# Kernel optimization log

Measured on AMD Instinct MI355X. Metric: run time of the kernel, lower is better.

The kernel has to match this reference:

```python
import jax, jax.numpy as jnp
import numpy as np

B, N, C_IN, C_OUT, K, E = 32, 1024, 64, 64, 3, 16
H1, M1 = 16, 2  # hyperGNN_dim, middle_dim (same for fc and fc1)


def setup_inputs() -> dict:
    key = jax.random.key(0)
    ks = jax.random.split(key, 20)
    rn = lambda k, shape, s=1.0: jax.random.normal(k, shape, jnp.float32) * s
    return {
        "x": rn(ks[0], (B, N, C_IN)),
        "node_emb0": rn(ks[1], (B, N, E)),
        "node_emb1": rn(ks[2], (N, E)),
        "time": rn(ks[3], (B, N, 1)),
        "day": rn(ks[4], (B, N, 1)),
        "speed": rn(ks[5], (B, N, 1)),
        "occupy": rn(ks[6], (B, N, 1)),
        # fc: dim_in -> 16 -> 2 -> embed_dim
        "fc_w1": rn(ks[7], (H1, C_IN), 0.1), "fc_b1": jnp.zeros((H1,), jnp.float32),
        "fc_w2": rn(ks[8], (M1, H1), 0.1), "fc_b2": jnp.zeros((M1,), jnp.float32),
        "fc_w3": rn(ks[9], (E, M1), 0.1), "fc_b3": jnp.zeros((E,), jnp.float32),
        # fc1: 1 -> 16 -> 2 -> embed_dim
        "fc1_w1": rn(ks[10], (H1, 1), 0.1), "fc1_b1": jnp.zeros((H1,), jnp.float32),
        "fc1_w2": rn(ks[11], (M1, H1), 0.1), "fc1_b2": jnp.zeros((M1,), jnp.float32),
        "fc1_w3": rn(ks[12], (E, M1), 0.1), "fc1_b3": jnp.zeros((E,), jnp.float32),
        "alpha": jnp.array([0.6], jnp.float32),
        "beta": jnp.array([0.4], jnp.float32),
        "weights_pool": rn(ks[13], (E, K, C_IN, C_OUT), 0.02),
        "backward_weights_pool": rn(ks[14], (E, K, C_IN, C_OUT), 0.02),
        "bias_pool": rn(ks[15], (E, C_OUT), 0.02),
        "weights1": rn(ks[16], (C_IN, C_OUT), 0.02),
        "att_w": rn(ks[17], (1, C_IN), 0.1),
        "att_b": jnp.zeros((1,), jnp.float32),
    }


def _mlp(x, w1, b1, w2, b2, w3, b3):
    h = jax.nn.sigmoid(x @ w1.T + b1)
    h = jax.nn.sigmoid(h @ w2.T + b2)
    return h @ w3.T + b3


def _attn_pool(xg, att_w, att_b, weights1):
    # xg: [B, K, N, C]
    nf = xg.mean(axis=1)                       # [B, N, C]
    scores = nf @ att_w.T + att_b              # [B, N, 1]
    aw = jax.nn.softmax(scores, axis=1)        # softmax over nodes
    gf = jnp.sum(nf * aw, axis=1)              # [B, C]
    return (gf @ weights1)[:, None, :]         # [B, 1, C_OUT], broadcasts over N


def reference(x, node_emb0, node_emb1, time, day, speed, occupy,
              fc_w1, fc_b1, fc_w2, fc_b2, fc_w3, fc_b3,
              fc1_w1, fc1_b1, fc1_w2, fc1_b2, fc1_w3, fc1_b3,
              alpha, beta, weights_pool, backward_weights_pool,
              bias_pool, weights1, att_w, att_b):
    k_steps = weights_pool.shape[1]
    # hypernetwork filters
    filt = _mlp(x, fc_w1, fc_b1, fc_w2, fc_b2, fc_w3, fc_b3)           # [B,N,E]
    f1 = _mlp(speed, fc1_w1, fc1_b1, fc1_w2, fc1_b2, fc1_w3, fc1_b3)   # [B,N,E]
    f2 = _mlp(occupy, fc1_w1, fc1_b1, fc1_w2, fc1_b2, fc1_w3, fc1_b3)  # [B,N,E]
    nv = jnp.tanh(node_emb0 * filt)
    nv = jnp.tanh(nv * f1)
    nv = jnp.tanh(nv * f2)
    supports = jax.nn.relu(jnp.einsum('bme,bne->bmn', nv, nv))          # [B,N,N]
    # forward diffusion
    xs = [x]
    for _ in range(1, k_steps):
        xs.append(jax.nn.leaky_relu(jnp.einsum('bmn,bnc->bmc', supports, xs[-1])))
    xg1 = jnp.stack(xs, axis=1)                                         # [B,K,N,C]
    gf = _attn_pool(xg1, att_w, att_b, weights1)                        # [B,1,O]
    w_fwd = jnp.einsum('ne,ekio->nkio', node_emb1, weights_pool)        # [N,K,C,O]
    # backward diffusion (starts from last forward step, uses A^T)
    s_t = jnp.swapaxes(supports, 1, 2)
    xb = [xs[-1]]
    for _ in range(1, k_steps):
        xb.append(jax.nn.leaky_relu(jnp.einsum('bmn,bnc->bmc', s_t, xb[-1])))
    xg2 = jnp.stack(xb, axis=1)                                         # [B,K,N,C]
    gf1 = _attn_pool(xg2, att_w, att_b, weights1)                       # [B,1,O]
    w_bwd = jnp.einsum('ne,ekio->nkio', node_emb1, backward_weights_pool)
    bias = node_emb1 @ bias_pool                                        # [N,O]
    d1 = jnp.einsum('bkni,nkio->bno', xg1, w_fwd)
    d2 = jnp.einsum('bkni,nkio->bno', xg2, w_bwd)
    return alpha * d1 + beta * d2 + bias + gf + gf1
```

## Files before the change

### kernel.cpp

```cpp
#include <hip/hip_runtime.h>
#include <cmath>

#define NB 32
#define NN 1024
#define NC 64
#define NE 16

typedef _Float16 f16;
typedef __attribute__((ext_vector_type(2))) _Float16 f16x2;
typedef __attribute__((ext_vector_type(4))) _Float16 f16x4;
typedef __attribute__((ext_vector_type(8))) _Float16 f16x8;
typedef __attribute__((ext_vector_type(16))) float f32x16;

#define NVSTR 24
#define SSTR  40
#define XSTR  40
#define ASTR  40

__device__ __forceinline__ float sigm(float v) { return 1.0f / (1.0f + expf(-v)); }
__device__ __forceinline__ float lrelu(float v) { return v > 0.0f ? v : 0.01f * v; }

__global__ __launch_bounds__(64) void nv_kernel(
    const float* __restrict__ x, const float* __restrict__ emb0,
    const float* __restrict__ speed, const float* __restrict__ occupy,
    const float* __restrict__ fw1, const float* __restrict__ fb1,
    const float* __restrict__ fw2, const float* __restrict__ fb2,
    const float* __restrict__ fw3, const float* __restrict__ fb3,
    const float* __restrict__ gw1, const float* __restrict__ gb1,
    const float* __restrict__ gw2, const float* __restrict__ gb2,
    const float* __restrict__ gw3, const float* __restrict__ gb3,
    float* __restrict__ nv_out)
{
    const int row = blockIdx.x * 64 + threadIdx.x;

    float h1[16];
    #pragma unroll
    for (int j = 0; j < 16; ++j) h1[j] = fb1[j];
    {
        const float4* xr = reinterpret_cast<const float4*>(x + (size_t)row * 64);
        #pragma unroll
        for (int i4 = 0; i4 < 16; ++i4) {
            float4 xv = xr[i4];
            #pragma unroll
            for (int j = 0; j < 16; ++j) {
                const float* wr = fw1 + j * 64 + i4 * 4;
                h1[j] += xv.x * wr[0] + xv.y * wr[1] + xv.z * wr[2] + xv.w * wr[3];
            }
        }
    }
    #pragma unroll
    for (int j = 0; j < 16; ++j) h1[j] = sigm(h1[j]);

    float h2a = fb2[0], h2b = fb2[1];
    #pragma unroll
    for (int j = 0; j < 16; ++j) { h2a += h1[j] * fw2[j]; h2b += h1[j] * fw2[16 + j]; }
    h2a = sigm(h2a); h2b = sigm(h2b);

    const float sp = speed[row], oc = occupy[row];
    float ga = gb2[0], gb_ = gb2[1];
    float oa = gb2[0], ob_ = gb2[1];
    #pragma unroll
    for (int j = 0; j < 16; ++j) {
        float g1 = sigm(sp * gw1[j] + gb1[j]);
        float o1 = sigm(oc * gw1[j] + gb1[j]);
        ga += g1 * gw2[j];  gb_ += g1 * gw2[16 + j];
        oa += o1 * gw2[j];  ob_ += o1 * gw2[16 + j];
    }
    ga = sigm(ga); gb_ = sigm(gb_); oa = sigm(oa); ob_ = sigm(ob_);

    const float* e0 = emb0 + (size_t)row * 16;
    float vout[16];
    #pragma unroll
    for (int j = 0; j < 16; ++j) {
        float filt = h2a * fw3[j * 2] + h2b * fw3[j * 2 + 1] + fb3[j];
        float f1v  = ga  * gw3[j * 2] + gb_ * gw3[j * 2 + 1] + gb3[j];
        float f2v  = oa  * gw3[j * 2] + ob_ * gw3[j * 2 + 1] + gb3[j];
        float v = tanhf(e0[j] * filt);
        v = tanhf(v * f1v);
        v = tanhf(v * f2v);
        vout[j] = v;
    }
    float4* dst = reinterpret_cast<float4*>(nv_out + (size_t)row * 16);
    #pragma unroll
    for (int q = 0; q < 4; ++q) {
        float4 o; o.x = vout[4 * q]; o.y = vout[4 * q + 1]; o.z = vout[4 * q + 2]; o.w = vout[4 * q + 3];
        dst[q] = o;
    }
}

__global__ __launch_bounds__(256) void xsplit_kernel(
    const float* __restrict__ x, f16* __restrict__ Th, f16* __restrict__ Tl)
{
    const int b = blockIdx.x;
    const int n0 = blockIdx.y * 64;
    const int t = threadIdx.x;

    __shared__ float tile[64][65];
    {
        int r = t >> 2;
        const float4* src = reinterpret_cast<const float4*>(x + ((size_t)b * NN + n0 + r) * NC);
        #pragma unroll
        for (int i = 0; i < 4; ++i) {
            int fi = (t & 3) + 4 * i;
            float4 vv = src[fi];
            tile[r][fi * 4 + 0] = vv.x; tile[r][fi * 4 + 1] = vv.y;
            tile[r][fi * 4 + 2] = vv.z; tile[r][fi * 4 + 3] = vv.w;
        }
    }
    __syncthreads();
    const int c = t & 63, ng = (t >> 6) * 16;
    f16x8 ph0, ph1, pl0, pl1;
    #pragma unroll
    for (int j = 0; j < 8; ++j) {
        float v = tile[ng + j][c];
        f16 h = (f16)v; ph0[j] = h; pl0[j] = (f16)(v - (float)h);
    }
    #pragma unroll
    for (int j = 0; j < 8; ++j) {
        float v = tile[ng + 8 + j][c];
        f16 h = (f16)v; ph1[j] = h; pl1[j] = (f16)(v - (float)h);
    }
    f16* dh = Th + ((size_t)b * NC + c) * NN + n0 + ng;
    f16* dl = Tl + ((size_t)b * NC + c) * NN + n0 + ng;
    *(f16x8*)dh = ph0; *(f16x8*)(dh + 8) = ph1;
    *(f16x8*)dl = pl0; *(f16x8*)(dl + 8) = pl1;
}

__global__ __launch_bounds__(512, 2) void sgen_fused_kernel(
    const float* __restrict__ nv,
    const f16* __restrict__ xTh, const f16* __restrict__ xTl,
    f16* __restrict__ Sh, f16* __restrict__ Sl,
    float* __restrict__ yout, f16* __restrict__ yTh, f16* __restrict__ yTl)
{
    const int b = blockIdx.x;
    const int m0 = blockIdx.y * 128;
    const int t = threadIdx.x;
    const int l = t & 63;
    const int g = l >> 5;
    const int l31 = l & 31;
    const int w = t >> 6;
    const int mq = w >> 1;
    const int nh = w & 1;

    __shared__ __align__(16) f16 nvBh[128 * NVSTR], nvBl[128 * NVSTR];
    __shared__ __align__(16) f16 Xsh[4][64 * XSTR], Xsl[4][64 * XSTR];
    __shared__ __align__(16) f16 Sth[4][128 * SSTR], Stl[4][128 * SSTR];

    const size_t sbase = (size_t)b * NN * NN;

    {
        int row = t >> 2, e0 = (t & 3) * 4;
        const float* src = nv + ((size_t)b * NN + m0 + row) * NE + e0;
        float v0 = src[0], v1 = src[1], v2 = src[2], v3 = src[3];
        f16x4 ph, pl;
        ph[0] = (f16)v0; pl[0] = (f16)(v0 - (float)ph[0]);
        ph[1] = (f16)v1; pl[1] = (f16)(v1 - (float)ph[1]);
        ph[2] = (f16)v2; pl[2] = (f16)(v2 - (float)ph[2]);
        ph[3] = (f16)v3; pl[3] = (f16)(v3 - (float)ph[3]);
        *(f16x4*)&Sth[0][row * NVSTR + e0] = ph;
        *(f16x4*)&Stl[0][row * NVSTR + e0] = pl;
    }
    __syncthreads();
    f16x8 Ah = *(const f16x8*)&Sth[0][(mq * 32 + l31) * NVSTR + g * 8];
    f16x8 Al = *(const f16x8*)&Stl[0][(mq * 32 + l31) * NVSTR + g * 8];

    f32x16 acc0, acc1;
    #pragma unroll
    for (int r = 0; r < 16; ++r) { acc0[r] = 0.0f; acc1[r] = 0.0f; }

    const int brow = t >> 2, be0 = (t & 3) * 4;
    const int xc = t >> 3, xpart = t & 7;
    const int xsub = xpart >> 1, xhalf = xpart & 1;

    for (int it = 0; it < 8; ++it) {
        {
            const float* src = nv + ((size_t)b * NN + it * 128 + brow) * NE + be0;
            float v0 = src[0], v1 = src[1], v2 = src[2], v3 = src[3];
            f16x4 ph, pl;
            ph[0] = (f16)v0; pl[0] = (f16)(v0 - (float)ph[0]);
            ph[1] = (f16)v1; pl[1] = (f16)(v1 - (float)ph[1]);
            ph[2] = (f16)v2; pl[2] = (f16)(v2 - (float)ph[2]);
            ph[3] = (f16)v3; pl[3] = (f16)(v3 - (float)ph[3]);
            *(f16x4*)&nvBh[brow * NVSTR + be0] = ph;
            *(f16x4*)&nvBl[brow * NVSTR + be0] = pl;
        }
        {
            const f16* sH = xTh + ((size_t)b * NC + xc) * NN + it * 128 + xsub * 32 + xhalf * 16;
            const f16* sL = xTl + ((size_t)b * NC + xc) * NN + it * 128 + xsub * 32 + xhalf * 16;
            *(f16x8*)&Xsh[xsub][xc * XSTR + xhalf * 16] = *(const f16x8*)sH;
            *(f16x8*)&Xsh[xsub][xc * XSTR + xhalf * 16 + 8] = *(const f16x8*)(sH + 8);
            *(f16x8*)&Xsl[xsub][xc * XSTR + xhalf * 16] = *(const f16x8*)sL;
            *(f16x8*)&Xsl[xsub][xc * XSTR + xhalf * 16 + 8] = *(const f16x8*)(sL + 8);
        }
        __syncthreads();

        #pragma unroll
        for (int tl = 0; tl < 2; ++tl) {
            const int tile = nh * 2 + tl;
            f16x8 Bh = *(const f16x8*)&nvBh[(tile * 32 + l31) * NVSTR + g * 8];
            f16x8 Bl = *(const f16x8*)&nvBl[(tile * 32 + l31) * NVSTR + g * 8];
            f32x16 sa;
            #pragma unroll
            for (int r = 0; r < 16; ++r) sa[r] = 0.0f;
            sa = __builtin_amdgcn_mfma_f32_32x32x16_f16(Al, Bh, sa, 0, 0, 0);
            sa = __builtin_amdgcn_mfma_f32_32x32x16_f16(Ah, Bl, sa, 0, 0, 0);
            sa = __builtin_amdgcn_mfma_f32_32x32x16_f16(Ah, Bh, sa, 0, 0, 0);
            const int n = it * 128 + tile * 32 + l31;
            #pragma unroll
            for (int r = 0; r < 16; ++r) {
                float vv = fmaxf(sa[r], 0.0f);
                f16 h = (f16)vv; f16 lo = (f16)(vv - (float)h);
                int mloc = mq * 32 + (r & 3) + 8 * (r >> 2) + 4 * g;
                Sh[sbase + (size_t)(m0 + mloc) * NN + n] = h;
                Sl[sbase + (size_t)(m0 + mloc) * NN + n] = lo;
                Sth[tile][mloc * SSTR + l31] = h;
                Stl[tile][mloc * SSTR + l31] = lo;
            }
        }
        __syncthreads();

        #pragma unroll
        for (int tl = 0; tl < 2; ++tl) {
            const int tile = nh * 2 + tl;
            #pragma unroll
            for (int ku = 0; ku < 2; ++ku) {
                f16x8 Ah2 = *(const f16x8*)&Sth[tile][(mq * 32 + l31) * SSTR + ku * 16 + g * 8];
                f16x8 Al2 = *(const f16x8*)&Stl[tile][(mq * 32 + l31) * SSTR + ku * 16 + g * 8];
                {
                    f16x8 Bh = *(const f16x8*)&Xsh[tile][l31 * XSTR + ku * 16 + g * 8];
                    f16x8 Bl = *(const f16x8*)&Xsl[tile][l31 * XSTR + ku * 16 + g * 8];
                    acc0 = __builtin_amdgcn_mfma_f32_32x32x16_f16(Al2, Bh, acc0, 0, 0, 0);
                    acc0 = __builtin_amdgcn_mfma_f32_32x32x16_f16(Ah2, Bl, acc0, 0, 0, 0);
                    acc0 = __builtin_amdgcn_mfma_f32_32x32x16_f16(Ah2, Bh, acc0, 0, 0, 0);
                }
                {
                    f16x8 Bh = *(const f16x8*)&Xsh[tile][(32 + l31) * XSTR + ku * 16 + g * 8];
                    f16x8 Bl = *(const f16x8*)&Xsl[tile][(32 + l31) * XSTR + ku * 16 + g * 8];
                    acc1 = __builtin_amdgcn_mfma_f32_32x32x16_f16(Al2, Bh, acc1, 0, 0, 0);
                    acc1 = __builtin_amdgcn_mfma_f32_32x32x16_f16(Ah2, Bl, acc1, 0, 0, 0);
                    acc1 = __builtin_amdgcn_mfma_f32_32x32x16_f16(Ah2, Bh, acc1, 0, 0, 0);
                }
            }
        }
        __syncthreads();
    }

    float* red = reinterpret_cast<float*>(&Sth[0][0]);
    if (nh == 1) {
        #pragma unroll
        for (int r = 0; r < 16; ++r) {
            int crow = (r & 3) + 8 * (r >> 2) + 4 * g;
            red[((mq * 2 + 0) * 32 + crow) * 33 + l31] = acc0[r];
            red[((mq * 2 + 1) * 32 + crow) * 33 + l31] = acc1[r];
        }
    }
    __syncthreads();
    if (nh == 0) {
        #pragma unroll
        for (int ch = 0; ch < 2; ++ch) {
            const int colg = ch * 32 + l31;
            #pragma unroll
            for (int q = 0; q < 4; ++q) {
                float v[4];
                #pragma unroll
                for (int j = 0; j < 4; ++j) {
                    int r = q * 4 + j;
                    int crow = j + 8 * q + 4 * g;
                    float part = (ch == 0) ? acc0[r] : acc1[r];
                    v[j] = lrelu(part + red[((mq * 2 + ch) * 32 + crow) * 33 + l31]);
                }
                const int mrow = m0 + mq * 32 + 8 * q + 4 * g;
                #pragma unroll
                for (int j = 0; j < 4; ++j)
                    yout[((size_t)b * NN + mrow + j) * NC + colg] = v[j];
                f16x4 ph, pl;
                #pragma unroll
                for (int j = 0; j < 4; ++j) {
                    f16 h = (f16)v[j];
                    ph[j] = h; pl[j] = (f16)(v[j] - (float)h);
                }
                *(f16x4*)&yTh[((size_t)b * NC + colg) * NN + mrow] = ph;
                *(f16x4*)&yTl[((size_t)b * NC + colg) * NN + mrow] = pl;
            }
        }
    }
}

__global__ __launch_bounds__(256) void diffuse5_kernel(
    const f16* __restrict__ Sh, const f16* __restrict__ Sl,
    const f16* __restrict__ xTh, const f16* __restrict__ xTl,
    float* __restrict__ yout, f16* __restrict__ yTh, f16* __restrict__ yTl,
    int writeT)
{
    const int b = blockIdx.x;
    const int m0 = blockIdx.y * 64;
    const int t = threadIdx.x;
    const int l = t & 63;
    const int g = l >> 5;
    const int l31 = l & 31;
    const int w = t >> 6;
    const int mh = w & 1;
    const int ch = w >> 1;

    __shared__ __align__(16) f16 As_h[2][64 * ASTR], As_l[2][64 * ASTR];
    __shared__ __align__(16) f16 Xs_h[2][64 * XSTR], Xs_l[2][64 * XSTR];

    const int arow = t >> 2, akc = t & 3;
    const f16* Ah_src = Sh + (size_t)b * NN * NN + (size_t)(m0 + arow) * NN + akc * 8;
    const f16* Al_src = Sl + (size_t)b * NN * NN + (size_t)(m0 + arow) * NN + akc * 8;
    const f16* Xh_src = xTh + ((size_t)b * NC + arow) * NN + akc * 8;
    const f16* Xl_src = xTl + ((size_t)b * NC + arow) * NN + akc * 8;

#define D5STAGE(n0v, bufv) do { \
    *(f16x8*)&As_h[bufv][arow * ASTR + akc * 8] = *(const f16x8*)(Ah_src + (n0v)); \
    *(f16x8*)&As_l[bufv][arow * ASTR + akc * 8] = *(const f16x8*)(Al_src + (n0v)); \
    *(f16x8*)&Xs_h[bufv][arow * XSTR + akc * 8] = *(const f16x8*)(Xh_src + (n0v)); \
    *(f16x8*)&Xs_l[bufv][arow * XSTR + akc * 8] = *(const f16x8*)(Xl_src + (n0v)); \
} while (0)

#define D5MFMA(bufv) do { \
    _Pragma("unroll") \
    for (int ku = 0; ku < 2; ++ku) { \
        f16x8 Bh = *(const f16x8*)&Xs_h[bufv][(ch * 32 + l31) * XSTR + ku * 16 + g * 8]; \
        f16x8 Bl = *(const f16x8*)&Xs_l[bufv][(ch * 32 + l31) * XSTR + ku * 16 + g * 8]; \
        f16x8 Ah = *(const f16x8*)&As_h[bufv][(mh * 32 + l31) * ASTR + ku * 16 + g * 8]; \
        f16x8 Al = *(const f16x8*)&As_l[bufv][(mh * 32 + l31) * ASTR + ku * 16 + g * 8]; \
        acc = __builtin_amdgcn_mfma_f32_32x32x16_f16(Al, Bh, acc, 0, 0, 0); \
        acc = __builtin_amdgcn_mfma_f32_32x32x16_f16(Ah, Bl, acc, 0, 0, 0); \
        acc = __builtin_amdgcn_mfma_f32_32x32x16_f16(Ah, Bh, acc, 0, 0, 0); \
    } \
} while (0)

    f32x16 acc;
    #pragma unroll
    for (int r = 0; r < 16; ++r) acc[r] = 0.0f;

    D5STAGE(0, 0);
    __syncthreads();

    for (int s = 0; s < 32; ++s) {
        const int cur = s & 1;
        if (s + 1 < 32) D5STAGE((s + 1) * 32, cur ^ 1);
        D5MFMA(cur);
        __syncthreads();
    }
#undef D5STAGE
#undef D5MFMA

    const int colg = ch * 32 + l31;
    #pragma unroll
    for (int q = 0; q < 4; ++q) {
        float v[4];
        #pragma unroll
        for (int j = 0; j < 4; ++j) {
            int r = q * 4 + j;
            v[j] = lrelu(acc[r]);
        }
        const int mrow = m0 + mh * 32 + 8 * q + 4 * g;
        #pragma unroll
        for (int j = 0; j < 4; ++j)
            yout[((size_t)b * NN + mrow + j) * NC + colg] = v[j];
        if (writeT) {
            f16x4 ph, pl;
            #pragma unroll
            for (int j = 0; j < 4; ++j) {
                f16 h = (f16)v[j];
                ph[j] = h; pl[j] = (f16)(v[j] - (float)h);
            }
            *(f16x4*)&yTh[((size_t)b * NC + colg) * NN + mrow] = ph;
            *(f16x4*)&yTl[((size_t)b * NC + colg) * NN + mrow] = pl;
        }
    }
}

__global__ __launch_bounds__(256) void diffuse_mfma_kernel(
    const float* __restrict__ nv, const float* __restrict__ xin,
    float* __restrict__ yout)
{
    const int b = blockIdx.x;
    const int m0 = blockIdx.y * 128;
    const int t = threadIdx.x;
    const int l = t & 63;
    const int w = t >> 6;
    const int g = l >> 5;
    const int l31 = l & 31;

    __shared__ __align__(16) f16 nvA_h[128 * NVSTR], nvA_l[128 * NVSTR];
    __shared__ __align__(16) f16 nvB_h[2][32 * NVSTR], nvB_l[2][32 * NVSTR];
    __shared__ __align__(16) f16 xT_h[2][64 * XSTR], xT_l[2][64 * XSTR];
    __shared__ __align__(16) f16 S_h[128 * SSTR], S_l[128 * SSTR];

    {
        int row = t >> 1, e0 = (t & 1) * 8;
        const float* src = nv + ((size_t)b * NN + m0 + row) * NE + e0;
        #pragma unroll
        for (int q = 0; q < 4; ++q) {
            float v0 = src[2 * q], v1 = src[2 * q + 1];
            f16 h0 = (f16)v0, h1 = (f16)v1;
            f16 lo0 = (f16)(v0 - (float)h0), lo1 = (f16)(v1 - (float)h1);
            f16x2 ph; ph[0] = h0; ph[1] = h1;
            f16x2 pl; pl[0] = lo0; pl[1] = lo1;
            *(f16x2*)&nvA_h[row * NVSTR + e0 + 2 * q] = ph;
            *(f16x2*)&nvA_l[row * NVSTR + e0 + 2 * q] = pl;
        }
    }

#define STAGE(n0v, bufv) do { \
    if (t < 64) { \
        int nl_ = t >> 1, e0_ = (t & 1) * 8; \
        const float* s_ = nv + ((size_t)b * NN + (n0v) + nl_) * NE + e0_; \
        _Pragma("unroll") \
        for (int q = 0; q < 4; ++q) { \
            float v0 = s_[2 * q], v1 = s_[2 * q + 1]; \
            f16 h0 = (f16)v0, h1 = (f16)v1; \
            f16 lo0 = (f16)(v0 - (float)h0), lo1 = (f16)(v1 - (float)h1); \
            f16x2 ph; ph[0] = h0; ph[1] = h1; \
            f16x2 pl; pl[0] = lo0; pl[1] = lo1; \
            *(f16x2*)&nvB_h[bufv][nl_ * NVSTR + e0_ + 2 * q] = ph; \
            *(f16x2*)&nvB_l[bufv][nl_ * NVSTR + e0_ + 2 * q] = pl; \
        } \
    } \
    { \
        int k_ = t >> 3, c0_ = t & 7; \
        const float* s_ = xin + ((size_t)b * NN + (n0v) + k_) * NC + c0_; \
        _Pragma("unroll") \
        for (int i = 0; i < 8; ++i) { \
            float v = s_[8 * i]; \
            f16 h = (f16)v; f16 lo = (f16)(v - (float)h); \
            int c_ = c0_ + 8 * i; \
            xT_h[bufv][c_ * XSTR + k_] = h; \
            xT_l[bufv][c_ * XSTR + k_] = lo; \
        } \
    } \
} while (0)

    STAGE(0, 0);
    __syncthreads();

    f32x16 acc0, acc1;
    #pragma unroll
    for (int r = 0; r < 16; ++r) { acc0[r] = 0.0f; acc1[r] = 0.0f; }

    const int mh = w & 1;
    const int cc = w >> 1;

    for (int s = 0; s < 32; ++s) {
        const int cur = s & 1;
        {
            f16x8 Ah = *(const f16x8*)&nvA_h[(w * 32 + l31) * NVSTR + g * 8];
            f16x8 Al = *(const f16x8*)&nvA_l[(w * 32 + l31) * NVSTR + g * 8];
            f16x8 Bh = *(const f16x8*)&nvB_h[cur][l31 * NVSTR + g * 8];
            f16x8 Bl = *(const f16x8*)&nvB_l[cur][l31 * NVSTR + g * 8];
            f32x16 sa;
            #pragma unroll
            for (int r = 0; r < 16; ++r) sa[r] = 0.0f;
            sa = __builtin_amdgcn_mfma_f32_32x32x16_f16(Al, Bh, sa, 0, 0, 0);
            sa = __builtin_amdgcn_mfma_f32_32x32x16_f16(Ah, Bl, sa, 0, 0, 0);
            sa = __builtin_amdgcn_mfma_f32_32x32x16_f16(Ah, Bh, sa, 0, 0, 0);
            #pragma unroll
            for (int r = 0; r < 16; ++r) {
                float vv = fmaxf(sa[r], 0.0f);
                f16 h = (f16)vv; f16 lo = (f16)(vv - (float)h);
                int row = w * 32 + (r & 3) + 8 * (r >> 2) + 4 * g;
                S_h[row * SSTR + l31] = h;
                S_l[row * SSTR + l31] = lo;
            }
        }
        if (s + 1 < 32) STAGE((s + 1) * 32, cur ^ 1);
        __syncthreads();
        #pragma unroll
        for (int chh = 0; chh < 2; ++chh) {
            f16x8 Bh = *(const f16x8*)&xT_h[cur][(cc * 32 + l31) * XSTR + chh * 16 + g * 8];
            f16x8 Bl = *(const f16x8*)&xT_l[cur][(cc * 32 + l31) * XSTR + chh * 16 + g * 8];
            {
                int sr = (mh * 64 + l31) * SSTR + chh * 16 + g * 8;
                f16x8 Ah = *(const f16x8*)&S_h[sr];
                f16x8 Al = *(const f16x8*)&S_l[sr];
                acc0 = __builtin_amdgcn_mfma_f32_32x32x16_f16(Al, Bh, acc0, 0, 0, 0);
                acc0 = __builtin_amdgcn_mfma_f32_32x32x16_f16(Ah, Bl, acc0, 0, 0, 0);
                acc0 = __builtin_amdgcn_mfma_f32_32x32x16_f16(Ah, Bh, acc0, 0, 0, 0);
            }
            {
                int sr = (mh * 64 + 32 + l31) * SSTR + chh * 16 + g * 8;
                f16x8 Ah = *(const f16x8*)&S_h[sr];
                f16x8 Al = *(const f16x8*)&S_l[sr];
                acc1 = __builtin_amdgcn_mfma_f32_32x32x16_f16(Al, Bh, acc1, 0, 0, 0);
                acc1 = __builtin_amdgcn_mfma_f32_32x32x16_f16(Ah, Bl, acc1, 0, 0, 0);
                acc1 = __builtin_amdgcn_mfma_f32_32x32x16_f16(Ah, Bh, acc1, 0, 0, 0);
            }
        }
        __syncthreads();
    }
#undef STAGE

    const int colg = cc * 32 + l31;
    #pragma unroll
    for (int r = 0; r < 16; ++r) {
        int row0 = m0 + mh * 64 + (r & 3) + 8 * (r >> 2) + 4 * g;
        yout[((size_t)b * NN + row0) * NC + colg] = lrelu(acc0[r]);
        yout[((size_t)b * NN + row0 + 32) * NC + colg] = lrelu(acc1[r]);
    }
}

__global__ __launch_bounds__(256) void scores_kernel(
    const float* __restrict__ x, const float* __restrict__ xs1, const float* __restrict__ xs2,
    const float* __restrict__ xb1, const float* __restrict__ xb2,
    const float* __restrict__ att_w, const float* __restrict__ att_b,
    float* __restrict__ sc)
{
    const int lane = threadIdx.x & 63;
    const int w = threadIdx.x >> 6;
    const int r = blockIdx.x * 4 + w;
    const int which = r >= NB * NN;
    const int rr = r - which * NB * NN;

    const float* p0 = which ? xs2 : x;
    const float* p1 = which ? xb1 : xs1;
    const float* p2 = which ? xb2 : xs2;

    size_t idx = (size_t)rr * NC + lane;
    float nf = (p0[idx] + p1[idx] + p2[idx]) * (1.0f / 3.0f);
    float v = nf * att_w[lane];
    #pragma unroll
    for (int off = 32; off > 0; off >>= 1) v += __shfl_xor(v, off);
    if (lane == 0) sc[r] = v + att_b[0];
}

__global__ __launch_bounds__(256) void softmax_kernel(float* __restrict__ sc)
{
    const int wb = blockIdx.x;
    const int t = threadIdx.x;
    const int lane = t & 63;
    const int w = t >> 6;
    float* p = sc + (size_t)wb * NN;

    __shared__ float red[4];
    float4 v = reinterpret_cast<const float4*>(p)[t];
    float m = fmaxf(fmaxf(v.x, v.y), fmaxf(v.z, v.w));
    #pragma unroll
    for (int off = 32; off > 0; off >>= 1) m = fmaxf(m, __shfl_xor(m, off));
    if (lane == 0) red[w] = m;
    __syncthreads();
    m = fmaxf(fmaxf(red[0], red[1]), fmaxf(red[2], red[3]));
    __syncthreads();
    v.x = expf(v.x - m); v.y = expf(v.y - m); v.z = expf(v.z - m); v.w = expf(v.w - m);
    float s = v.x + v.y + v.z + v.w;
    #pragma unroll
    for (int off = 32; off > 0; off >>= 1) s += __shfl_xor(s, off);
    if (lane == 0) red[w] = s;
    __syncthreads();
    const float inv = 1.0f / (red[0] + red[1] + red[2] + red[3]);
    v.x *= inv; v.y *= inv; v.z *= inv; v.w *= inv;
    reinterpret_cast<float4*>(p)[t] = v;
}

__global__ __launch_bounds__(256) void poolpart_kernel(
    const float* __restrict__ x, const float* __restrict__ xs1, const float* __restrict__ xs2,
    const float* __restrict__ xb1, const float* __restrict__ xb2,
    const float* __restrict__ sc, float* __restrict__ partial)
{
    const int chunk = blockIdx.x;
    const int b = blockIdx.y;
    const int which = blockIdx.z;
    const int lane = threadIdx.x & 63;
    const int w = threadIdx.x >> 6;

    const float* p0 = which ? xs2 : x;
    const float* p1 = which ? xb1 : xs1;
    const float* p2 = which ? xb2 : xs2;

    const int n0 = chunk * 64;
    const size_t base = (size_t)b * NN;
    float acc = 0.0f;
    for (int j = w; j < 64; j += 4) {
        int n = n0 + j;
        size_t idx = (base + n) * NC + lane;
        float nf = (p0[idx] + p1[idx] + p2[idx]) * (1.0f / 3.0f);
        acc += nf * sc[((size_t)which * NB + b) * NN + n];
    }
    __shared__ float red[4][64];
    red[w][lane] = acc;
    __syncthreads();
    if (w == 0) {
        float s = red[0][lane] + red[1][lane] + red[2][lane] + red[3][lane];
        partial[(((size_t)which * NB + b) * 16 + chunk) * 64 + lane] = s;
    }
}

__global__ __launch_bounds__(256) void poolfin_kernel(
    const float* __restrict__ partial, const float* __restrict__ w1,
    float* __restrict__ gf_out)
{
    const int wb = blockIdx.x;
    const int t = threadIdx.x;
    const int lane = t & 63;
    const int w = t >> 6;

    __shared__ float red[4][64];
    __shared__ float gfin[64];
    float acc = 0.0f;
    #pragma unroll
    for (int r = w; r < 16; r += 4)
        acc += partial[((size_t)wb * 16 + r) * 64 + lane];
    red[w][lane] = acc;
    __syncthreads();
    if (w == 0) gfin[lane] = red[0][lane] + red[1][lane] + red[2][lane] + red[3][lane];
    __syncthreads();
    if (w == 0) {
        float s = 0.0f;
        #pragma unroll
        for (int c = 0; c < 64; ++c) s += gfin[c] * w1[c * 64 + lane];
        gf_out[(size_t)wb * 64 + lane] = s;
    }
}

__global__ __launch_bounds__(256) void wbuild_both_kernel(
    const float* __restrict__ emb1, const float* __restrict__ wpf,
    const float* __restrict__ wpb, float* __restrict__ Wf, float* __restrict__ Wb)
{
    const int ki = blockIdx.x;
    const int chunk = blockIdx.y;
    const int which = blockIdx.z;
    const float* pool = which ? wpb : wpf;
    float* W = which ? Wb : Wf;
    const int t = threadIdx.x;
    const int o = t & 63;

    __shared__ float slab[16][64];
    __shared__ float eloc[256][16];

    for (int idx = t; idx < 1024; idx += 256)
        slab[idx >> 6][idx & 63] = pool[((size_t)(idx >> 6) * 192 + ki) * 64 + (idx & 63)];
    for (int idx = t; idx < 4096; idx += 256)
        eloc[idx >> 4][idx & 15] = emb1[((size_t)chunk * 256 + (idx >> 4)) * 16 + (idx & 15)];
    __syncthreads();
    for (int nl = t >> 6; nl < 256; nl += 4) {
        float s = 0.0f;
        #pragma unroll
        for (int e = 0; e < 16; ++e) s += eloc[nl][e] * slab[e][o];
        W[((size_t)(chunk * 256 + nl) * 192 + ki) * 64 + o] = s;
    }
}

__global__ __launch_bounds__(256) void apply_both_kernel(
    const float* __restrict__ Wf, const float* __restrict__ Wb,
    const float* __restrict__ emb1, const float* __restrict__ bias_pool,
    const float* __restrict__ x, const float* __restrict__ xs1, const float* __restrict__ xs2,
    const float* __restrict__ xb1, const float* __restrict__ xb2,
    const float* __restrict__ gf, const float* __restrict__ alpha, const float* __restrict__ beta,
    float* __restrict__ out)
{
    const int n = blockIdx.x;
    const int t = threadIdx.x;
    const int o = t & 63;
    const int bg = t >> 6;

    __shared__ float Xs[5][32][64];
    __shared__ float e1s[16];

    if (t < 16) e1s[t] = emb1[n * 16 + t];
    const float* srcs[5] = {x, xs1, xs2, xb1, xb2};
    #pragma unroll
    for (int k = 0; k < 5; ++k) {
        const float* sp = srcs[k];
        #pragma unroll
        for (int r = 0; r < 2; ++r) {
            int idx = t + 256 * r;
            int b = idx >> 4, i4 = idx & 15;
            reinterpret_cast<float4*>(&Xs[k][b][0])[i4] =
                reinterpret_cast<const float4*>(sp + ((size_t)b * NN + n) * NC)[i4];
        }
    }
    __syncthreads();

    const float* wfp = Wf + (size_t)n * 192 * 64 + o;
    const float* wbp = Wb + (size_t)n * 192 * 64 + o;

    float accf[8] = {}, accb[8] = {};
    #pragma unroll 4
    for (int k4 = 0; k4 < 48; ++k4) {
        const int ki0 = k4 * 4;
        const int k = ki0 >> 6;
        const int i0 = ki0 & 63;
        float wf0 = wfp[(size_t)(ki0 + 0) * 64], wf1 = wfp[(size_t)(ki0 + 1) * 64];
        float wf2 = wfp[(size_t)(ki0 + 2) * 64], wf3 = wfp[(size_t)(ki0 + 3) * 64];
        float wb0 = wbp[(size_t)(ki0 + 0) * 64], wb1 = wbp[(size_t)(ki0 + 1) * 64];
        float wb2 = wbp[(size_t)(ki0 + 2) * 64], wb3 = wbp[(size_t)(ki0 + 3) * 64];
        #pragma unroll
        for (int j = 0; j < 8; ++j) {
            int bb = bg * 8 + j;
            float4 xf = *reinterpret_cast<const float4*>(&Xs[k][bb][i0]);
            accf[j] += xf.x * wf0 + xf.y * wf1 + xf.z * wf2 + xf.w * wf3;
            float4 xb = *reinterpret_cast<const float4*>(&Xs[2 + k][bb][i0]);
            accb[j] += xb.x * wb0 + xb.y * wb1 + xb.z * wb2 + xb.w * wb3;
        }
    }

    float bias_o = 0.0f;
    #pragma unroll
    for (int e = 0; e < 16; ++e) bias_o += e1s[e] * bias_pool[e * 64 + o];
    const float al = alpha[0], be = beta[0];
    #pragma unroll
    for (int j = 0; j < 8; ++j) {
        int b = bg * 8 + j;
        float g = gf[(size_t)b * 64 + o] + gf[((size_t)NB + b) * 64 + o];
        out[((size_t)b * NN + n) * NC + o] = al * accf[j] + be * accb[j] + bias_o + g;
    }
}

__global__ __launch_bounds__(256) void wbuild_kernel(
    const float* __restrict__ emb1, const float* __restrict__ pool,
    float* __restrict__ W)
{
    const int ki = blockIdx.x;
    const int chunk = blockIdx.y;
    const int t = threadIdx.x;
    const int o = t & 63;

    __shared__ float slab[16][64];
    __shared__ float eloc[256][16];

    for (int idx = t; idx < 1024; idx += 256)
        slab[idx >> 6][idx & 63] = pool[((size_t)(idx >> 6) * 192 + ki) * 64 + (idx & 63)];
    for (int idx = t; idx < 4096; idx += 256)
        eloc[idx >> 4][idx & 15] = emb1[((size_t)chunk * 256 + (idx >> 4)) * 16 + (idx & 15)];
    __syncthreads();
    for (int nl = t >> 6; nl < 256; nl += 4) {
        float s = 0.0f;
        #pragma unroll
        for (int e = 0; e < 16; ++e) s += eloc[nl][e] * slab[e][o];
        W[((size_t)(chunk * 256 + nl) * 192 + ki) * 64 + o] = s;
    }
}

__global__ __launch_bounds__(256) void apply_kernel(
    const float* __restrict__ W, const float* __restrict__ emb1,
    const float* __restrict__ bias_pool,
    const float* __restrict__ s0, const float* __restrict__ s1, const float* __restrict__ s2,
    const float* __restrict__ gf, const float* __restrict__ scale,
    float* __restrict__ out, int pass)
{
    const int n = blockIdx.x;
    const int t = threadIdx.x;
    const int o = t & 63;
    const int bg = t >> 6;

    __shared__ float Wn[192][64];
    __shared__ float Xs[3][32][64];
    __shared__ float e1s[16];

    if (t < 16) e1s[t] = emb1[n * 16 + t];
    {
        const float4* src = reinterpret_cast<const float4*>(W + (size_t)n * 192 * 64);
        float4* dst = reinterpret_cast<float4*>(&Wn[0][0]);
        #pragma unroll
        for (int r = 0; r < 12; ++r) dst[t + 256 * r] = src[t + 256 * r];
    }
    const float* srcs[3] = {s0, s1, s2};
    #pragma unroll
    for (int k = 0; k < 3; ++k) {
        const float* sp = srcs[k];
        #pragma unroll
        for (int r = 0; r < 2; ++r) {
            int idx = t + 256 * r;
            int b = idx >> 4, i4 = idx & 15;
            reinterpret_cast<float4*>(&Xs[k][b][0])[i4] =
                reinterpret_cast<const float4*>(sp + ((size_t)b * NN + n) * NC)[i4];
        }
    }
    __syncthreads();

    float acc[8] = {};
    #pragma unroll 4
    for (int ki = 0; ki < 192; ++ki) {
        float wv = Wn[ki][o];
        int k = ki >> 6, i = ki & 63;
        #pragma unroll
        for (int j = 0; j < 8; ++j) acc[j] += Xs[k][bg * 8 + j][i] * wv;
    }

    const float sc = scale[0];
    if (pass == 0) {
        float bias_o = 0.0f;
        #pragma unroll
        for (int e = 0; e < 16; ++e) bias_o += e1s[e] * bias_pool[e * 64 + o];
        #pragma unroll
        for (int j = 0; j < 8; ++j) {
            int b = bg * 8 + j;
            float g = gf[(size_t)b * 64 + o] + gf[((size_t)NB + b) * 64 + o];
            out[((size_t)b * NN + n) * NC + o] = sc * acc[j] + bias_o + g;
        }
    } else {
        #pragma unroll
        for (int j = 0; j < 8; ++j) {
            int b = bg * 8 + j;
            out[((size_t)b * NN + n) * NC + o] += sc * acc[j];
        }
    }
}

__global__ __launch_bounds__(256) void final_kernel(
    const float* __restrict__ emb1,
    const float* __restrict__ wpf, const float* __restrict__ wpb,
    const float* __restrict__ bias_pool,
    const float* __restrict__ x, const float* __restrict__ xs1, const float* __restrict__ xs2,
    const float* __restrict__ xb1, const float* __restrict__ xb2,
    const float* __restrict__ gf, const float* __restrict__ alpha, const float* __restrict__ beta,
    float* __restrict__ out)
{
    const int n = blockIdx.x;
    const int t = threadIdx.x;
    const int o = t & 63;
    const int bg = t >> 6;

    __shared__ float Wk[64][64];
    __shared__ float xk[32][64];
    __shared__ float e1[16];
    if (t < 16) e1[t] = emb1[n * 16 + t];

    float acc[2][8];
    #pragma unroll
    for (int d = 0; d < 2; ++d)
        #pragma unroll
        for (int j = 0; j < 8; ++j) acc[d][j] = 0.0f;

    const float* srcs[2][3] = {{x, xs1, xs2}, {xs2, xb1, xb2}};

    #pragma unroll
    for (int dir = 0; dir < 2; ++dir) {
        const float* wp = dir ? wpb : wpf;
        #pragma unroll
        for (int k = 0; k < 3; ++k) {
            __syncthreads();
            for (int idx = t; idx < 4096; idx += 256) {
                int i = idx >> 6, oo = idx & 63;
                float s = 0.0f;
                #pragma unroll
                for (int e = 0; e < 16; ++e) s += e1[e] * wp[(((size_t)e * 3 + k) * 64 + i) * 64 + oo];
                Wk[i][oo] = s;
            }
            const float* src = srcs[dir][k];
            for (int idx = t; idx < 2048; idx += 256) {
                int bb = idx >> 6, ii = idx & 63;
                xk[bb][ii] = src[((size_t)bb * NN + n) * NC + ii];
            }
            __syncthreads();
            #pragma unroll
            for (int j = 0; j < 8; ++j) {
                int bb = bg * 8 + j;
                float s = 0.0f;
                #pragma unroll
                for (int i = 0; i < 64; i += 4) {
                    float4 xv = *reinterpret_cast<const float4*>(&xk[bb][i]);
                    s += xv.x * Wk[i][o] + xv.y * Wk[i + 1][o] + xv.z * Wk[i + 2][o] + xv.w * Wk[i + 3][o];
                }
                acc[dir][j] += s;
            }
        }
    }

    float bias_o = 0.0f;
    #pragma unroll
    for (int e = 0; e < 16; ++e) bias_o += e1[e] * bias_pool[e * 64 + o];
    const float al = alpha[0], be = beta[0];
    #pragma unroll
    for (int j = 0; j < 8; ++j) {
        int bb = bg * 8 + j;
        float g = gf[(size_t)bb * 64 + o] + gf[((size_t)NB + bb) * 64 + o];
        out[((size_t)bb * NN + n) * NC + o] = al * acc[0][j] + be * acc[1][j] + bias_o + g;
    }
}

__global__ __launch_bounds__(256) void attnpool_kernel(
    const float* __restrict__ a0, const float* __restrict__ a1, const float* __restrict__ a2,
    const float* __restrict__ c0, const float* __restrict__ c1, const float* __restrict__ c2,
    const float* __restrict__ att_w, const float* __restrict__ att_b,
    const float* __restrict__ w1, float* __restrict__ gf_out)
{
    const int b = blockIdx.x;
    const int which = blockIdx.y;
    const float* p0 = which ? c0 : a0;
    const float* p1 = which ? c1 : a1;
    const float* p2 = which ? c2 : a2;
    const int t = threadIdx.x;
    const int lane = t & 63;
    const int w = t >> 6;

    __shared__ float sc[NN];
    __shared__ float red[4];
    __shared__ float gfp[4][64];
    __shared__ float gfin[64];

    const float aw = att_w[lane];
    const size_t base = (size_t)b * NN * NC;

    for (int n = w; n < NN; n += 4) {
        size_t idx = base + (size_t)n * NC + lane;
        float nf = (p0[idx] + p1[idx] + p2[idx]) * (1.0f / 3.0f);
        float v = nf * aw;
        #pragma unroll
        for (int off = 32; off > 0; off >>= 1) v += __shfl_xor(v, off);
        if (lane == 0) sc[n] = v + att_b[0];
    }
    __syncthreads();
    float m = -INFINITY;
    for (int i = t; i < NN; i += 256) m = fmaxf(m, sc[i]);
    #pragma unroll
    for (int off = 32; off > 0; off >>= 1) m = fmaxf(m, __shfl_xor(m, off));
    if (lane == 0) red[w] = m;
    __syncthreads();
    m = fmaxf(fmaxf(red[0], red[1]), fmaxf(red[2], red[3]));
    __syncthreads();
    float s = 0.0f;
    for (int i = t; i < NN; i += 256) { float e = expf(sc[i] - m); sc[i] = e; s += e; }
    #pragma unroll
    for (int off = 32; off > 0; off >>= 1) s += __shfl_xor(s, off);
    if (lane == 0) red[w] = s;
    __syncthreads();
    const float inv_denom = 1.0f / (red[0] + red[1] + red[2] + red[3]);

    float acc = 0.0f;
    for (int n = w; n < NN; n += 4) {
        size_t idx = base + (size_t)n * NC + lane;
        float nf = (p0[idx] + p1[idx] + p2[idx]) * (1.0f / 3.0f);
        acc += nf * sc[n];
    }
    gfp[w][lane] = acc;
    __syncthreads();
    if (w == 0) gfin[lane] = (gfp[0][lane] + gfp[1][lane] + gfp[2][lane] + gfp[3][lane]) * inv_denom;
    __syncthreads();
    if (w == 0) {
        float s2 = 0.0f;
        #pragma unroll
        for (int c = 0; c < 64; ++c) s2 += gfin[c] * w1[c * 64 + lane];
        gf_out[((size_t)which * NB + b) * 64 + lane] = s2;
    }
}

extern "C" void kernel_launch(void* const* d_in, const int* in_sizes, int n_in,
                              void* d_out, int out_size, void* d_ws, size_t ws_size,
                              hipStream_t stream)
{
    const float* x      = (const float*)d_in[0];
    const float* emb0   = (const float*)d_in[1];
    const float* emb1   = (const float*)d_in[2];
    const float* speed  = (const float*)d_in[5];
    const float* occupy = (const float*)d_in[6];
    const float* fw1 = (const float*)d_in[7];
    const float* fb1 = (const float*)d_in[8];
    const float* fw2 = (const float*)d_in[9];
    const float* fb2 = (const float*)d_in[10];
    const float* fw3 = (const float*)d_in[11];
    const float* fb3 = (const float*)d_in[12];
    const float* gw1 = (const float*)d_in[13];
    const float* gb1 = (const float*)d_in[14];
    const float* gw2 = (const float*)d_in[15];
    const float* gb2 = (const float*)d_in[16];
    const float* gw3 = (const float*)d_in[17];
    const float* gb3 = (const float*)d_in[18];
    const float* alpha = (const float*)d_in[19];
    const float* beta  = (const float*)d_in[20];
    const float* wpf = (const float*)d_in[21];
    const float* wpb = (const float*)d_in[22];
    const float* bias_pool = (const float*)d_in[23];
    const float* w1 = (const float*)d_in[24];
    const float* att_w = (const float*)d_in[25];
    const float* att_b = (const float*)d_in[26];
    float* out = (float*)d_out;

    float* ws = (float*)d_ws;
    float* nv  = ws;
    float* xs1 = nv + (size_t)NB * NN * NE;
    float* xs2 = xs1 + (size_t)NB * NN * NC;
    float* xb1 = xs2 + (size_t)NB * NN * NC;
    float* xb2 = xb1 + (size_t)NB * NN * NC;
    float* gfb = xb2 + (size_t)NB * NN * NC;
    float* scb = gfb + 4096;
    float* ppb = scb + (size_t)2 * NB * NN;
    float* Wbuf = ppb + (size_t)2 * NB * 16 * 64;
    f16* Sh = (f16*)(Wbuf + (size_t)NN * 192 * 64);
    f16* Sl = Sh + (size_t)NB * NN * NN;
    f16* T0h = Sl + (size_t)NB * NN * NN;
    f16* T0l = T0h + (size_t)NB * NC * NN;
    f16* T1h = T0l + (size_t)NB * NC * NN;
    f16* T1l = T1h + (size_t)NB * NC * NN;
    float* WbufB = (float*)Sh;

    const size_t base_elems = (size_t)NB * NN * NE + 4 * (size_t)NB * NN * NC + 4096;
    const size_t attn_elems = (size_t)2 * NB * NN + (size_t)2 * NB * 16 * 64;
    const size_t w_elems = (size_t)NN * 192 * 64;
    const size_t need_mid = (base_elems + attn_elems + w_elems) * sizeof(float);
    const size_t need_full = need_mid +
        ((size_t)2 * NB * NN * NN + (size_t)4 * NB * NC * NN) * sizeof(f16);

    hipLaunchKernelGGL(nv_kernel, dim3(NB * NN / 64), dim3(64), 0, stream,
                       x, emb0, speed, occupy, fw1, fb1, fw2, fb2, fw3, fb3,
                       gw1, gb1, gw2, gb2, gw3, gb3, nv);

    if (ws_size >= need_full) {
        hipLaunchKernelGGL(xsplit_kernel, dim3(NB, NN / 64), dim3(256), 0, stream, x, T0h, T0l);
        hipLaunchKernelGGL(sgen_fused_kernel, dim3(NB, NN / 128), dim3(512), 0, stream,
                           nv, T0h, T0l, Sh, Sl, xs1, T1h, T1l);
        dim3 gd5(NB, NN / 64);
        hipLaunchKernelGGL(diffuse5_kernel, gd5, dim3(256), 0, stream,
                           Sh, Sl, T1h, T1l, xs2, T0h, T0l, 1);
        hipLaunchKernelGGL(diffuse5_kernel, gd5, dim3(256), 0, stream,
                           Sh, Sl, T0h, T0l, xb1, T1h, T1l, 1);
        hipLaunchKernelGGL(diffuse5_kernel, gd5, dim3(256), 0, stream,
                           Sh, Sl, T1h, T1l, xb2, T0h, T0l, 0);
        hipLaunchKernelGGL(scores_kernel, dim3(2 * NB * NN / 4), dim3(256), 0, stream,
                           x, xs1, xs2, xb1, xb2, att_w, att_b, scb);
        hipLaunchKernelGGL(softmax_kernel, dim3(2 * NB), dim3(256), 0, stream, scb);
        hipLaunchKernelGGL(poolpart_kernel, dim3(16, NB, 2), dim3(256), 0, stream,
                           x, xs1, xs2, xb1, xb2, scb, ppb);
        hipLaunchKernelGGL(poolfin_kernel, dim3(2 * NB), dim3(256), 0, stream, ppb, w1, gfb);
        hipLaunchKernelGGL(wbuild_both_kernel, dim3(192, 4, 2), dim3(256), 0, stream,
                           emb1, wpf, wpb, Wbuf, WbufB);
        hipLaunchKernelGGL(apply_both_kernel, dim3(NN), dim3(256), 0, stream,
                           Wbuf, WbufB, emb1, bias_pool, x, xs1, xs2, xb1, xb2,
                           gfb, alpha, beta, out);
    } else if (ws_size >= need_mid) {
        dim3 gd(NB, NN / 128);
        hipLaunchKernelGGL(diffuse_mfma_kernel, gd, dim3(256), 0, stream, nv, x, xs1);
        hipLaunchKernelGGL(diffuse_mfma_kernel, gd, dim3(256), 0, stream, nv, xs1, xs2);
        hipLaunchKernelGGL(diffuse_mfma_kernel, gd, dim3(256), 0, stream, nv, xs2, xb1);
        hipLaunchKernelGGL(diffuse_mfma_kernel, gd, dim3(256), 0, stream, nv, xb1, xb2);
        hipLaunchKernelGGL(scores_kernel, dim3(2 * NB * NN / 4), dim3(256), 0, stream,
                           x, xs1, xs2, xb1, xb2, att_w, att_b, scb);
        hipLaunchKernelGGL(softmax_kernel, dim3(2 * NB), dim3(256), 0, stream, scb);
        hipLaunchKernelGGL(poolpart_kernel, dim3(16, NB, 2), dim3(256), 0, stream,
                           x, xs1, xs2, xb1, xb2, scb, ppb);
        hipLaunchKernelGGL(poolfin_kernel, dim3(2 * NB), dim3(256), 0, stream, ppb, w1, gfb);
        hipLaunchKernelGGL(wbuild_kernel, dim3(192, 4), dim3(256), 0, stream, emb1, wpf, Wbuf);
        hipLaunchKernelGGL(apply_kernel, dim3(NN), dim3(256), 0, stream,
                           Wbuf, emb1, bias_pool, x, xs1, xs2, gfb, alpha, out, 0);
        hipLaunchKernelGGL(wbuild_kernel, dim3(192, 4), dim3(256), 0, stream, emb1, wpb, Wbuf);
        hipLaunchKernelGGL(apply_kernel, dim3(NN), dim3(256), 0, stream,
                           Wbuf, emb1, bias_pool, xs2, xb1, xb2, gfb, beta, out, 1);
    } else {
        dim3 gd(NB, NN / 128);
        hipLaunchKernelGGL(diffuse_mfma_kernel, gd, dim3(256), 0, stream, nv, x, xs1);
        hipLaunchKernelGGL(diffuse_mfma_kernel, gd, dim3(256), 0, stream, nv, xs1, xs2);
        hipLaunchKernelGGL(diffuse_mfma_kernel, gd, dim3(256), 0, stream, nv, xs2, xb1);
        hipLaunchKernelGGL(diffuse_mfma_kernel, gd, dim3(256), 0, stream, nv, xb1, xb2);
        hipLaunchKernelGGL(attnpool_kernel, dim3(NB, 2), dim3(256), 0, stream,
                           x, xs1, xs2, xs2, xb1, xb2, att_w, att_b, w1, gfb);
        hipLaunchKernelGGL(final_kernel, dim3(NN), dim3(256), 0, stream,
                           emb1, wpf, wpb, bias_pool, x, xs1, xs2, xb1, xb2, gfb, alpha, beta, out);
    }
}
```

Measured before the change: 289.9 us.

## Use split-fp16 MFMA for the per-node weight apply kernel

Replaces the scalar FMA loop in the per-node apply kernel with 32x32x16 fp16 MFMA instructions. It keeps fp32-level accuracy by splitting each operand into high and low fp16 parts and issuing three MFMAs per step. Each wave handles one direction (forward or backward) and one 32-column output half. The backward partial sums are passed through shared memory to be combined with the forward ones. This cuts ALU work, at the cost of extra conversion instructions and strided scalar loads of W when building the B fragments.

New measurement: 245.9 us. -15.2%, faster.

```diff
diff --git a/kernel.cpp b/kernel.cpp
--- a/kernel.cpp
+++ b/kernel.cpp
@@ -16,6 +16,7 @@
 #define SSTR  40
 #define XSTR  40
 #define ASTR  40
+#define A5STR 72
 
 __device__ __forceinline__ float sigm(float v) { return 1.0f / (1.0f + expf(-v)); }
 __device__ __forceinline__ float lrelu(float v) { return v > 0.0f ? v : 0.01f * v; }
@@ -642,7 +643,7 @@
     }
 }
 
-__global__ __launch_bounds__(256) void apply_both_kernel(
+__global__ __launch_bounds__(256) void apply_mfma_kernel(
     const float* __restrict__ Wf, const float* __restrict__ Wb,
     const float* __restrict__ emb1, const float* __restrict__ bias_pool,
     const float* __restrict__ x, const float* __restrict__ xs1, const float* __restrict__ xs2,
@@ -652,59 +653,83 @@
 {
     const int n = blockIdx.x;
     const int t = threadIdx.x;
-    const int o = t & 63;
-    const int bg = t >> 6;
-
-    __shared__ float Xs[5][32][64];
+    const int l = t & 63;
+    const int g = l >> 5;
+    const int l31 = l & 31;
+    const int w = t >> 6;
+    const int dir = w >> 1;
+    const int ot  = w & 1;
+
+    __shared__ __align__(16) f16 A5h[5][32 * A5STR], A5l[5][32 * A5STR];
     __shared__ float e1s[16];
 
     if (t < 16) e1s[t] = emb1[n * 16 + t];
+
     const float* srcs[5] = {x, xs1, xs2, xb1, xb2};
-    #pragma unroll
-    for (int k = 0; k < 5; ++k) {
-        const float* sp = srcs[k];
-        #pragma unroll
-        for (int r = 0; r < 2; ++r) {
-            int idx = t + 256 * r;
-            int b = idx >> 4, i4 = idx & 15;
-            reinterpret_cast<float4*>(&Xs[k][b][0])[i4] =
-                reinterpret_cast<const float4*>(sp + ((size_t)b * NN + n) * NC)[i4];
-        }
-    }
-    __syncthreads();
-
-    const float* wfp = Wf + (size_t)n * 192 * 64 + o;
-    const float* wbp = Wb + (size_t)n * 192 * 64 + o;
-
-    float accf[8] = {}, accb[8] = {};
-    #pragma unroll 4
-    for (int k4 = 0; k4 < 48; ++k4) {
-        const int ki0 = k4 * 4;
-        const int k = ki0 >> 6;
-        const int i0 = ki0 & 63;
-        float wf0 = wfp[(size_t)(ki0 + 0) * 64], wf1 = wfp[(size_t)(ki0 + 1) * 64];
-        float wf2 = wfp[(size_t)(ki0 + 2) * 64], wf3 = wfp[(size_t)(ki0 + 3) * 64];
-        float wb0 = wbp[(size_t)(ki0 + 0) * 64], wb1 = wbp[(size_t)(ki0 + 1) * 64];
-        float wb2 = wbp[(size_t)(ki0 + 2) * 64], wb3 = wbp[(size_t)(ki0 + 3) * 64];
+    for (int idx = t; idx < 5 * 32 * 16; idx += 256) {
+        int s = idx / (32 * 16);
+        int rem = idx - s * (32 * 16);
+        int b = rem >> 4, i4 = rem & 15;
+        float4 v = *reinterpret_cast<const float4*>(srcs[s] + ((size_t)b * NN + n) * NC + i4 * 4);
+        f16x4 ph, pl;
+        ph[0] = (f16)v.x; pl[0] = (f16)(v.x - (float)ph[0]);
+        ph[1] = (f16)v.y; pl[1] = (f16)(v.y - (float)ph[1]);
+        ph[2] = (f16)v.z; pl[2] = (f16)(v.z - (float)ph[2]);
+        ph[3] = (f16)v.w; pl[3] = (f16)(v.w - (float)ph[3]);
+        *(f16x4*)&A5h[s][b * A5STR + i4 * 4] = ph;
+        *(f16x4*)&A5l[s][b * A5STR + i4 * 4] = pl;
+    }
+    __syncthreads();
+
+    const float* W = dir ? Wb : Wf;
+    const float* wbase = W + (size_t)n * 192 * 64 + ot * 32 + l31;
+
+    f32x16 acc;
+    #pragma unroll
+    for (int r = 0; r < 16; ++r) acc[r] = 0.0f;
+
+    #pragma unroll 3
+    for (int c = 0; c < 12; ++c) {
+        const int ki0 = c * 16;
+        const int s = dir * 2 + (ki0 >> 6);
+        const int iloc = (ki0 & 63) + g * 8;
+        f16x8 Ah = *(const f16x8*)&A5h[s][l31 * A5STR + iloc];
+        f16x8 Al = *(const f16x8*)&A5l[s][l31 * A5STR + iloc];
+        f16x8 Bh, Bl;
         #pragma unroll
         for (int j = 0; j < 8; ++j) {
-            int bb = bg * 8 + j;
-            float4 xf = *reinterpret_cast<const float4*>(&Xs[k][bb][i0]);
-            accf[j] += xf.x * wf0 + xf.y * wf1 + xf.z * wf2 + xf.w * wf3;
-            float4 xb = *reinterpret_cast<const float4*>(&Xs[2 + k][bb][i0]);
-            accb[j] += xb.x * wb0 + xb.y * wb1 + xb.z * wb2 + xb.w * wb3;
-        }
-    }
-
-    float bias_o = 0.0f;
-    #pragma unroll
-    for (int e = 0; e < 16; ++e) bias_o += e1s[e] * bias_pool[e * 64 + o];
-    const float al = alpha[0], be = beta[0];
-    #pragma unroll
-    for (int j = 0; j < 8; ++j) {
-        int b = bg * 8 + j;
-        float g = gf[(size_t)b * 64 + o] + gf[((size_t)NB + b) * 64 + o];
-        out[((size_t)b * NN + n) * NC + o] = al * accf[j] + be * accb[j] + bias_o + g;
+            float wv = wbase[(size_t)(ki0 + g * 8 + j) * 64];
+            f16 h = (f16)wv;
+            Bh[j] = h; Bl[j] = (f16)(wv - (float)h);
+        }
+        acc = __builtin_amdgcn_mfma_f32_32x32x16_f16(Al, Bh, acc, 0, 0, 0);
+        acc = __builtin_amdgcn_mfma_f32_32x32x16_f16(Ah, Bl, acc, 0, 0, 0);
+        acc = __builtin_amdgcn_mfma_f32_32x32x16_f16(Ah, Bh, acc, 0, 0, 0);
+    }
+
+    __syncthreads();
+    float* red = reinterpret_cast<float*>(&A5h[0][0]);
+    if (dir == 1) {
+        #pragma unroll
+        for (int r = 0; r < 16; ++r) {
+            int crow = (r & 3) + 8 * (r >> 2) + 4 * g;
+            red[(ot * 32 + crow) * 33 + l31] = acc[r];
+        }
+    }
+    __syncthreads();
+    if (dir == 0) {
+        const int o = ot * 32 + l31;
+        float bias_o = 0.0f;
+        #pragma unroll
+        for (int e = 0; e < 16; ++e) bias_o += e1s[e] * bias_pool[e * 64 + o];
+        const float al = alpha[0], be = beta[0];
+        #pragma unroll
+        for (int r = 0; r < 16; ++r) {
+            int b = (r & 3) + 8 * (r >> 2) + 4 * g;
+            float gv = gf[(size_t)b * 64 + o] + gf[((size_t)NB + b) * 64 + o];
+            out[((size_t)b * NN + n) * NC + o] =
+                al * acc[r] + be * red[(ot * 32 + b) * 33 + l31] + bias_o + gv;
+        }
     }
 }
 
@@ -1016,7 +1041,7 @@
         hipLaunchKernelGGL(poolfin_kernel, dim3(2 * NB), dim3(256), 0, stream, ppb, w1, gfb);
         hipLaunchKernelGGL(wbuild_both_kernel, dim3(192, 4, 2), dim3(256), 0, stream,
                            emb1, wpf, wpb, Wbuf, WbufB);
-        hipLaunchKernelGGL(apply_both_kernel, dim3(NN), dim3(256), 0, stream,
+        hipLaunchKernelGGL(apply_mfma_kernel, dim3(NN), dim3(256), 0, stream,
                            Wbuf, WbufB, emb1, bias_pool, x, xs1, xs2, xb1, xb2,
                            gfb, alpha, beta, out);
     } else if (ws_size >= need_mid) {
```
